# Optimization experiments

Measured on AMD Instinct MI355X. Metric: run time of the kernel, lower is better.

The kernel has to match this reference:

```python
import jax, jax.numpy as jnp
import numpy as np

N = 30000      # nodes
E = 480000     # edges
NF = 92        # node features
EF = 50        # edge features
D1 = 64        # dim1
D2 = 64        # dim2
L = 3          # conv_count
FC = 2         # fc_count
G = 256        # graphs in batch
EPS = 1e-5


def setup_inputs() -> dict:
    key = jax.random.key(0)
    ks = jax.random.split(key, 20)
    s = 0.05
    zd = 2 * D1 + EF  # CGConv concat dim
    inp = {
        "x": jax.random.normal(ks[0], (N, NF), jnp.float32),
        "edge_attr": jax.random.uniform(ks[1], (E, EF), jnp.float32),
        "lin0_w": jax.random.normal(ks[2], (NF, D1), jnp.float32) * s,
        "lin0_b": jnp.zeros((D1,), jnp.float32),
        "conv_wf": jax.random.normal(ks[3], (L, zd, D1), jnp.float32) * s,
        "conv_bf": jnp.zeros((L, D1), jnp.float32),
        "conv_ws": jax.random.normal(ks[4], (L, zd, D1), jnp.float32) * s,
        "conv_bs": jnp.zeros((L, D1), jnp.float32),
        "bn_gamma": jnp.ones((L, D1), jnp.float32),
        "bn_beta": jnp.zeros((L, D1), jnp.float32),
        "lin1_w": jax.random.normal(ks[5], (D1, D2), jnp.float32) * s,
        "lin1_b": jnp.zeros((D2,), jnp.float32),
        "fc_w": jax.random.normal(ks[6], (FC, D2, D2), jnp.float32) * s,
        "fc_b": jnp.zeros((FC, D2), jnp.float32),
        "lin2_w": jax.random.normal(ks[7], (D2, 1), jnp.float32) * s,
        "lin2_b": jnp.zeros((1,), jnp.float32),
        "edge_index": jax.random.randint(ks[8], (2, E), 0, N),
        "batch": jnp.sort(jax.random.randint(ks[9], (N,), 0, G)),
        "n_graphs": G,
    }
    return inp


def reference(x, edge_attr, lin0_w, lin0_b, conv_wf, conv_bf, conv_ws, conv_bs,
              bn_gamma, bn_beta, lin1_w, lin1_b, fc_w, fc_b, lin2_w, lin2_b,
              edge_index, batch, n_graphs):
    n = x.shape[0]
    src = edge_index[0]  # x_j (source)
    dst = edge_index[1]  # x_i (target, aggregation index)
    h = jax.nn.relu(x @ lin0_w + lin0_b)  # [N, D1]

    # per-target edge counts for mean aggregation (constant across layers)
    cnt = jax.ops.segment_sum(jnp.ones((src.shape[0],), h.dtype), dst, num_segments=n)
    cnt = jnp.maximum(cnt, 1.0)[:, None]

    for l in range(L):
        # z = [x_i || x_j || e_ij]  -> gated message sigmoid(Wf z) * softplus(Ws z)
        z = jnp.concatenate([h[dst], h[src], edge_attr], axis=-1)  # [E, 2*D1+EF]
        m = jax.nn.sigmoid(z @ conv_wf[l] + conv_bf[l]) * jax.nn.softplus(z @ conv_ws[l] + conv_bs[l])
        aggr = jax.ops.segment_sum(m, dst, num_segments=n) / cnt  # mean aggr [N, D1]
        # BatchNorm (training-mode batch stats, biased variance as in torch)
        mu = jnp.mean(aggr, axis=0)
        var = jnp.var(aggr, axis=0)
        aggr = (aggr - mu) * jax.lax.rsqrt(var + EPS) * bn_gamma[l] + bn_beta[l]
        h = jax.nn.relu(h + aggr)  # residual then outer ReLU

    # global mean pool over graphs
    gcnt = jnp.maximum(jax.ops.segment_sum(jnp.ones((n,), h.dtype), batch, num_segments=n_graphs), 1.0)[:, None]
    out = jax.ops.segment_sum(h, batch, num_segments=n_graphs) / gcnt  # [G, D1]

    out = jax.nn.relu(out @ lin1_w + lin1_b)
    for f in range(FC):
        out = jax.nn.relu(out @ fc_w[f] + fc_b[f])
    out = out @ lin2_w + lin2_b
    return out.reshape(-1)  # [G]
```

## Files before the change

### kernel.cpp

```cpp
#include <hip/hip_runtime.h>
#include <hip/hip_bf16.h>

#define N_NODES 30000
#define N_EDGES 480000
#define NFEAT 92
#define EFEAT 50
#define D1 64
#define ZD 178
#define NL 3
#define NG 256
#define BN_EPS 1e-5f
#define NTILES (N_EDGES / 16)
#define EDGE_BLOCKS 7500
#define EDGE_GRID 7504

#define LIN0_BLOCKS 512
#define CNT_BLOCKS 1875
#define WPREP_BLOCKS 96
#define SCAN_BLOCKS ((N_NODES + 255) / 256)
#define BUILD_BLOCKS 1875
#define NP_BLOCKS 1024

typedef __attribute__((ext_vector_type(8))) short bf16x8;
typedef __attribute__((ext_vector_type(8))) unsigned short u16x8;
typedef __attribute__((ext_vector_type(4))) unsigned short u16x4;
typedef __attribute__((ext_vector_type(4))) float f32x4;

static __device__ __forceinline__ unsigned short f2bf(float v) {
  __hip_bfloat16 b = __float2bfloat16(v);
  return *(unsigned short*)&b;
}
static __device__ __forceinline__ float bfu(unsigned short u) {
  union { unsigned int i; float f; } c;
  c.i = ((unsigned int)u) << 16;
  return c.f;
}

static __device__ __forceinline__ void nodeproj_body(
    int blk0, int nblk, const float* __restrict__ hin, float* __restrict__ hout,
    const float* __restrict__ wfp, const float* __restrict__ wsm,
    unsigned short* __restrict__ projd_pk, unsigned short* __restrict__ projs_pk,
    const float* __restrict__ aggr, float* __restrict__ aggr_z,
    const float* __restrict__ invc, const float* __restrict__ musum,
    const float* __restrict__ sqsum, const float* __restrict__ gamma,
    const float* __restrict__ beta, int do_bn, float (*hl)[64]) {
  const int lane = threadIdx.x & 63;
  const int w = threadIdx.x >> 6;
  const float* W = (w < 2) ? wfp : wsm;
  const int roff = (w & 1) * 64;
  float wreg[D1];
#pragma unroll
  for (int k = 0; k < D1; ++k) wreg[k] = W[(size_t)(roff + k) * D1 + lane];
  unsigned short* pk = (w & 1) ? projs_pk : projd_pk;
  const int slot = (w < 2) ? 0 : 4;
  const int poff = (lane >> 2) * 8 + (lane & 3) + slot;
  float r = 0.0f, sh = 0.0f;
  if (do_bn) {
    const float mu = musum[lane] * (1.0f / N_NODES);
    const float var = sqsum[lane] * (1.0f / N_NODES) - mu * mu;
    r = gamma[lane] * rsqrtf(var + BN_EPS);
    sh = beta[lane] - mu * r;
  }
  for (int i = blk0; i < N_NODES; i += nblk) {
    float hv = hin[(size_t)i * D1 + lane];
    if (do_bn) {
      const float av = aggr[(size_t)i * D1 + lane] * invc[i];
      hv = fmaxf(hv + fmaf(av, r, sh), 0.0f);
      if (w == 0) hout[(size_t)i * D1 + lane] = hv;
    }
    if (w == 1) aggr_z[(size_t)i * D1 + lane] = 0.0f;
    hl[w][lane] = hv;
    __builtin_amdgcn_wave_barrier();
    const float4* hr = (const float4*)&hl[w][0];
    float acc = 0.0f;
#pragma unroll
    for (int k4 = 0; k4 < D1 / 4; ++k4) {
      const float4 v = hr[k4];
      acc = fmaf(v.x, wreg[4 * k4 + 0], acc);
      acc = fmaf(v.y, wreg[4 * k4 + 1], acc);
      acc = fmaf(v.z, wreg[4 * k4 + 2], acc);
      acc = fmaf(v.w, wreg[4 * k4 + 3], acc);
    }
    pk[(size_t)i * 128 + poff] = f2bf(acc);
    __builtin_amdgcn_wave_barrier();
  }
}

extern "C" __global__ void __launch_bounds__(256)
k_init(const float* __restrict__ x, const float* __restrict__ w,
       const float* __restrict__ b, float* __restrict__ h,
       const int* __restrict__ ei, int* __restrict__ cnt,
       const float* __restrict__ conv_wf, const float* __restrict__ conv_ws,
       unsigned short* __restrict__ Bp) {
  const int blk = blockIdx.x;
  if (blk < LIN0_BLOCKS) {
    const int lane = threadIdx.x & 63;
    const int wave = (blk * 256 + threadIdx.x) >> 6;
    const int nw = (LIN0_BLOCKS * 256) >> 6;
    float wreg[NFEAT];
#pragma unroll
    for (int k = 0; k < NFEAT; ++k) wreg[k] = w[k * D1 + lane];
    const float bj = b[lane];
    for (int i = wave; i < N_NODES; i += nw) {
      const float2* xr = (const float2*)(x + (size_t)i * NFEAT);
      float acc = bj;
#pragma unroll
      for (int k = 0; k < NFEAT / 2; ++k) {
        const float2 v = xr[k];
        acc = fmaf(v.x, wreg[2 * k], acc);
        acc = fmaf(v.y, wreg[2 * k + 1], acc);
      }
      h[(size_t)i * D1 + lane] = fmaxf(acc, 0.0f);
    }
  } else if (blk < LIN0_BLOCKS + CNT_BLOCKS) {
    const int e = (blk - LIN0_BLOCKS) * 256 + threadIdx.x;
    if (e < N_EDGES) atomicAdd(&cnt[ei[N_EDGES + e]], 1);
  } else {
    const int idx = (blk - LIN0_BLOCKS - CNT_BLOCKS) * 256 + threadIdx.x;
    const int j = idx & 7;
    const int lane = (idx >> 3) & 63;
    const int frag = (idx >> 9) & 15;
    const int l = idx >> 13;
    const int n = frag & 3;
    const int t = (frag >> 2) & 1;
    const int m = frag >> 3;
    const int k = t * 32 + (lane >> 4) * 8 + j;
    const int feat = (lane & 15) * 4 + n;
    float v = 0.0f;
    if (k < EFEAT) {
      const float* W = (m == 0) ? conv_wf : conv_ws;
      v = W[(size_t)l * ZD * D1 + (size_t)(128 + k) * D1 + feat];
    }
    Bp[idx] = f2bf(v);
  }
}

extern "C" __global__ void __launch_bounds__(256)
k_scan1(const int* __restrict__ cnt, int* __restrict__ lpre, int* __restrict__ ptot) {
  const int t = threadIdx.x;
  const int idx = blockIdx.x * 256 + t;
  const int v = (idx < N_NODES) ? cnt[idx] : 0;
  __shared__ int bs[256];
  bs[t] = v;
  __syncthreads();
  for (int off = 1; off < 256; off <<= 1) {
    int u = (t >= off) ? bs[t - off] : 0;
    __syncthreads();
    bs[t] += u;
    __syncthreads();
  }
  if (idx < N_NODES) lpre[idx] = bs[t] - v;
  if (t == 255) ptot[blockIdx.x] = bs[255];
}

extern "C" __global__ void __launch_bounds__(256)
k_scan23(const int* __restrict__ cnt, const int* __restrict__ lpre,
         const int* __restrict__ ptot, const int* __restrict__ batch,
         int* __restrict__ wptr, float* __restrict__ invc,
         int* __restrict__ grp) {
  __shared__ int bs[128];
  const int t = threadIdx.x;
  if (t < 128) bs[t] = (t < SCAN_BLOCKS) ? ptot[t] : 0;
  __syncthreads();
  for (int off = 1; off < 128; off <<= 1) {
    int u = 0;
    if (t < 128 && t >= off) u = bs[t - off];
    __syncthreads();
    if (t < 128 && t >= off) bs[t] += u;
    __syncthreads();
  }
  const int idx = blockIdx.x * 256 + t;
  if (idx >= N_NODES) return;
  const int bid = idx >> 8;
  const int boff = (bid == 0) ? 0 : bs[bid - 1];
  wptr[idx] = boff + lpre[idx];
  invc[idx] = 1.0f / fmaxf((float)cnt[idx], 1.0f);
  const int bt = batch[idx];
  if (idx == 0)
    for (int g = 0; g <= bt; ++g) grp[g] = 0;
  else {
    const int pb = batch[idx - 1];
    for (int g = pb + 1; g <= bt; ++g) grp[g] = idx;
  }
  if (idx == N_NODES - 1)
    for (int g = bt + 1; g <= NG; ++g) grp[g] = N_NODES;
}

extern "C" __global__ void __launch_bounds__(256)
k_build(const int* __restrict__ ei, int* __restrict__ wptr,
        int4* __restrict__ ds4, const float* __restrict__ ea,
        unsigned short* __restrict__ eapb,
        const float* __restrict__ h0, const float* __restrict__ wfl,
        const float* __restrict__ wsl, unsigned short* __restrict__ projd_pk,
        unsigned short* __restrict__ projs_pk, float* __restrict__ aggrA) {
  __shared__ float hl4[4][64];
  if (blockIdx.x >= BUILD_BLOCKS) {
    nodeproj_body(blockIdx.x - BUILD_BLOCKS, NP_BLOCKS, h0, nullptr, wfl, wsl,
                  projd_pk, projs_pk, nullptr, aggrA, nullptr, nullptr, nullptr,
                  nullptr, nullptr, 0, hl4);
    return;
  }
  const int e0 = blockIdx.x * 256;
  const int e = e0 + threadIdx.x;
  const int d = ei[N_EDGES + e];
  const int s = ei[e];
  const int pos = atomicAdd(&wptr[d], 1);

  const int l16 = threadIdx.x & 15;
  const int sub = threadIdx.x >> 4;
#pragma unroll
  for (int r = 0; r < 16; ++r) {
    const size_t ge = e0 + r * 16 + sub;
    unsigned short o0 = 0, o1 = 0, o2 = 0, o3 = 0;
    if (l16 < 12) {
      const float4 v = *(const float4*)(ea + ge * EFEAT + l16 * 4);
      o0 = f2bf(v.x); o1 = f2bf(v.y); o2 = f2bf(v.z); o3 = f2bf(v.w);
    } else if (l16 == 12) {
      const float2 v = *(const float2*)(ea + ge * EFEAT + 48);
      o0 = f2bf(v.x); o1 = f2bf(v.y);
    }
    u16x4 st;
    st[0] = o0; st[1] = o1; st[2] = o2; st[3] = o3;
    *(u16x4*)(eapb + (ge << 6) + l16 * 4) = st;
  }

  ds4[pos] = make_int4(d, s, e, 0);
}

extern "C" __global__ void __launch_bounds__(256)
k_nodeproj(const float* __restrict__ hin, float* __restrict__ hout,
           const float* __restrict__ wfp, const float* __restrict__ wsm,
           unsigned short* __restrict__ projd_pk, unsigned short* __restrict__ projs_pk,
           const float* __restrict__ aggr, float* __restrict__ aggr_z,
           const float* __restrict__ invc,
           const float* __restrict__ musum, const float* __restrict__ sqsum,
           const float* __restrict__ gamma, const float* __restrict__ beta) {
  __shared__ float hl[4][64];
  nodeproj_body(blockIdx.x, gridDim.x, hin, hout, wfp, wsm, projd_pk, projs_pk,
                aggr, aggr_z, invc, musum, sqsum, gamma, beta, 1, hl);
}

extern "C" __global__ void __launch_bounds__(256)
k_edgemm(const unsigned short* __restrict__ projd_pk,
         const unsigned short* __restrict__ projs_pk,
         const unsigned short* __restrict__ eapb,
         const int4* __restrict__ ds4,
         const unsigned short* __restrict__ Bp,
         const float* __restrict__ bfp, const float* __restrict__ bsp,
         float* __restrict__ aggr, float* __restrict__ musum,
         float* __restrict__ sqsum) {
  const int lane = threadIdx.x & 63;
  const int wv = threadIdx.x >> 6;
  const int col = lane & 15;
  const int quad = lane >> 4;
  __shared__ float mlds[4][16][68];

  const int vbid = (blockIdx.x & 7) * 938 + (blockIdx.x >> 3);
  if (blockIdx.x == 0 && wv == 0) {
    musum[lane] = 0.0f;
    sqsum[lane] = 0.0f;
  }
  if (vbid >= EDGE_BLOCKS) return;

  const int t = vbid * 4 + wv;
  const int base = t * 16;

  int dr[4], sr[4];
#pragma unroll
  for (int r = 0; r < 4; ++r) {
    const int4 q = ds4[base + quad * 4 + r];
    dr[r] = q.x;
    sr[r] = q.y;
  }
  const int oe = ds4[base + col].z;
  const bf16x8 Af0 = *(const bf16x8*)(eapb + ((size_t)oe << 6) + quad * 8);
  const bf16x8 Af1 = *(const bf16x8*)(eapb + ((size_t)oe << 6) + 32 + quad * 8);

  bf16x8 Bf[2][2][4];
#pragma unroll
  for (int m = 0; m < 2; ++m)
#pragma unroll
    for (int tt = 0; tt < 2; ++tt)
#pragma unroll
      for (int n = 0; n < 4; ++n)
        Bf[m][tt][n] = *(const bf16x8*)(Bp + ((((m * 2 + tt) * 4 + n) * 64 + lane) * 8));

  const f32x4 bf4 = *(const f32x4*)(bfp + col * 4);
  const f32x4 bs4 = *(const f32x4*)(bsp + col * 4);

  f32x4 aF[4], aS[4];
#pragma unroll
  for (int r = 0; r < 4; ++r) {
    const int d = dr[r];
    const int s = sr[r];
    const u16x8 pd = *(const u16x8*)(projd_pk + (size_t)d * 128 + col * 8);
    const u16x8 ss = *(const u16x8*)(projs_pk + (size_t)s * 128 + col * 8);
#pragma unroll
    for (int n = 0; n < 4; ++n) {
      aF[n][r] = bfu(pd[n]) + bfu(ss[n]) + bf4[n];
      aS[n][r] = bfu(pd[n + 4]) + bfu(ss[n + 4]) + bs4[n];
    }
  }

#pragma unroll
  for (int n = 0; n < 4; ++n) {
    aF[n] = __builtin_amdgcn_mfma_f32_16x16x32_bf16(Af0, Bf[0][0][n], aF[n], 0, 0, 0);
    aF[n] = __builtin_amdgcn_mfma_f32_16x16x32_bf16(Af1, Bf[0][1][n], aF[n], 0, 0, 0);
    aS[n] = __builtin_amdgcn_mfma_f32_16x16x32_bf16(Af0, Bf[1][0][n], aS[n], 0, 0, 0);
    aS[n] = __builtin_amdgcn_mfma_f32_16x16x32_bf16(Af1, Bf[1][1][n], aS[n], 0, 0, 0);
  }

#pragma unroll
  for (int r = 0; r < 4; ++r) {
    f32x4 mv;
#pragma unroll
    for (int n = 0; n < 4; ++n) {
      const float af = aF[n][r];
      const float as = aS[n][r];
      const float sg = __builtin_amdgcn_rcpf(1.0f + __expf(-af));
      const float sp = fmaxf(as, 0.0f) + __logf(1.0f + __expf(-fabsf(as)));
      mv[n] = sg * sp;
    }
    *(f32x4*)&mlds[wv][quad * 4 + r][col * 4] = mv;
  }
  __builtin_amdgcn_wave_barrier();

  float sum = 0.0f;
  int dcur = ds4[base].x;
#pragma unroll
  for (int p = 0; p < 16; ++p) {
    sum += mlds[wv][p][lane];
    const int dnxt = (p < 15) ? ds4[base + p + 1].x : -1;
    if (dnxt != dcur) {
      atomicAdd(&aggr[(size_t)dcur * D1 + lane], sum);
      sum = 0.0f;
      dcur = dnxt;
    }
  }
}

extern "C" __global__ void __launch_bounds__(256)
k_stats(const float* __restrict__ aggr, const float* __restrict__ invc,
        float* __restrict__ musum, float* __restrict__ sqsum) {
  const int j = threadIdx.x & 63;
  const int rid = (blockIdx.x * blockDim.x + threadIdx.x) >> 6;
  const int rstr = (gridDim.x * blockDim.x) >> 6;
  float s = 0.0f, sq = 0.0f;
  for (int i = rid; i < N_NODES; i += rstr) {
    const float v = aggr[(size_t)i * D1 + j] * invc[i];
    s += v;
    sq = fmaf(v, v, sq);
  }
  __shared__ float ls[256], lq[256];
  ls[threadIdx.x] = s;
  lq[threadIdx.x] = sq;
  __syncthreads();
  if (threadIdx.x < 64) {
    s = ls[j] + ls[64 + j] + ls[128 + j] + ls[192 + j];
    sq = lq[j] + lq[64 + j] + lq[128 + j] + lq[192 + j];
    atomicAdd(&musum[j], s);
    atomicAdd(&sqsum[j], sq);
  }
}

extern "C" __global__ void __launch_bounds__(256)
k_poolmlp(const float* __restrict__ h, const float* __restrict__ aggr,
          const float* __restrict__ invc,
          const float* __restrict__ musum, const float* __restrict__ sqsum,
          const float* __restrict__ gamma, const float* __restrict__ beta,
          const int* __restrict__ grp,
          const float* __restrict__ lin1_w, const float* __restrict__ lin1_b,
          const float* __restrict__ fc_w, const float* __restrict__ fc_b,
          const float* __restrict__ lin2_w, const float* __restrict__ lin2_b,
          float* __restrict__ out) {
  const int g = blockIdx.x;
  const int lane = threadIdx.x & 63;
  const int wv = threadIdx.x >> 6;
  const float mu = musum[lane] * (1.0f / N_NODES);
  const float var = sqsum[lane] * (1.0f / N_NODES) - mu * mu;
  const float r = gamma[lane] * rsqrtf(var + BN_EPS);
  const float sh = beta[lane] - mu * r;
  const int s = grp[g], e = grp[g + 1];
  float acc = 0.0f;
  for (int i = s + wv; i < e; i += 4) {
    const float hv = h[(size_t)i * D1 + lane];
    const float av = aggr[(size_t)i * D1 + lane] * invc[i];
    acc += fmaxf(hv + fmaf(av, r, sh), 0.0f);
  }
  __shared__ float red[4][64];
  __shared__ float vin[64];
  red[wv][lane] = acc;
  __syncthreads();
  const int j = threadIdx.x;
  float v = 0.0f;
  if (j < 64) {
    const float inv = 1.0f / fmaxf((float)(e - s), 1.0f);
    v = (red[0][j] + red[1][j] + red[2][j] + red[3][j]) * inv;
  }
  for (int layer = 0; layer < 3; ++layer) {
    if (j < 64) vin[j] = v;
    __syncthreads();
    if (j < 64) {
      const float* W;
      const float* B;
      if (layer == 0) {
        W = lin1_w;
        B = lin1_b;
      } else {
        W = fc_w + (size_t)(layer - 1) * D1 * D1;
        B = fc_b + (size_t)(layer - 1) * D1;
      }
      float a2 = B[j];
#pragma unroll 16
      for (int k = 0; k < D1; ++k) a2 = fmaf(vin[k], W[k * D1 + j], a2);
      v = fmaxf(a2, 0.0f);
    }
    __syncthreads();
  }
  if (j < 64) {
    float p = v * lin2_w[j];
#pragma unroll
    for (int off = 32; off > 0; off >>= 1) p += __shfl_down(p, off);
    if (j == 0) out[g] = p + lin2_b[0];
  }
}

extern "C" void kernel_launch(void* const* d_in, const int* in_sizes, int n_in,
                              void* d_out, int out_size, void* d_ws, size_t ws_size,
                              hipStream_t stream) {
  const float* x        = (const float*)d_in[0];
  const float* ea       = (const float*)d_in[1];
  const float* lin0_w   = (const float*)d_in[2];
  const float* lin0_b   = (const float*)d_in[3];
  const float* conv_wf  = (const float*)d_in[4];
  const float* conv_bf  = (const float*)d_in[5];
  const float* conv_ws  = (const float*)d_in[6];
  const float* conv_bs  = (const float*)d_in[7];
  const float* bn_gamma = (const float*)d_in[8];
  const float* bn_beta  = (const float*)d_in[9];
  const float* lin1_w   = (const float*)d_in[10];
  const float* lin1_b   = (const float*)d_in[11];
  const float* fc_w     = (const float*)d_in[12];
  const float* fc_b     = (const float*)d_in[13];
  const float* lin2_w   = (const float*)d_in[14];
  const float* lin2_b   = (const float*)d_in[15];
  const int*   ei       = (const int*)d_in[16];
  const int*   batch    = (const int*)d_in[17];

  uintptr_t p = (uintptr_t)d_ws;
  auto alloc = [&](size_t bytes) {
    p = (p + 255) & ~(size_t)255;
    void* r = (void*)p;
    p += bytes;
    return r;
  };
  float* h0     = (float*)alloc((size_t)N_NODES * 64 * 4);
  float* h1     = (float*)alloc((size_t)N_NODES * 64 * 4);
  unsigned short* projd_pk = (unsigned short*)alloc((size_t)N_NODES * 128 * 2);
  unsigned short* projs_pk = (unsigned short*)alloc((size_t)N_NODES * 128 * 2);
  float* aggrA  = (float*)alloc((size_t)N_NODES * 64 * 4);
  float* aggrB  = (float*)alloc((size_t)N_NODES * 64 * 4);
  float* musum  = (float*)alloc(128 * 4);
  float* sqsum  = musum + 64;
  float* invc   = (float*)alloc((size_t)N_NODES * 4);
  int*   cnt    = (int*)alloc((size_t)N_NODES * 4);
  int*   lpre   = (int*)alloc((size_t)N_NODES * 4);
  int*   ptot   = (int*)alloc((size_t)SCAN_BLOCKS * 4);
  int*   wptr   = (int*)alloc((size_t)N_NODES * 4);
  int4*  ds4    = (int4*)alloc((size_t)N_EDGES * 16);
  int*   grp    = (int*)alloc((size_t)(NG + 1) * 4);
  unsigned short* eapb = (unsigned short*)alloc((size_t)N_EDGES * 64 * 2);
  unsigned short* Bp   = (unsigned short*)alloc((size_t)NL * 16 * 64 * 8 * 2);

  hipMemsetAsync(cnt, 0, N_NODES * sizeof(int), stream);
  k_init<<<LIN0_BLOCKS + CNT_BLOCKS + WPREP_BLOCKS, 256, 0, stream>>>(
      x, lin0_w, lin0_b, h0, ei, cnt, conv_wf, conv_ws, Bp);
  k_scan1<<<SCAN_BLOCKS, 256, 0, stream>>>(cnt, lpre, ptot);
  k_scan23<<<SCAN_BLOCKS, 256, 0, stream>>>(cnt, lpre, ptot, batch, wptr, invc, grp);
  k_build<<<BUILD_BLOCKS + NP_BLOCKS, 256, 0, stream>>>(
      ei, wptr, ds4, ea, eapb, h0, conv_wf, conv_ws, projd_pk, projs_pk, aggrA);

  float* aggr_of[NL] = {aggrA, aggrB, aggrA};
  const float* hin_of[NL]  = {h0, h0, h1};
  float* hout_of[NL]       = {h0, h1, h0};

  for (int l = 0; l < NL; ++l) {
    const float* wfl = conv_wf + (size_t)l * ZD * D1;
    const float* wsl = conv_ws + (size_t)l * ZD * D1;
    if (l > 0)
      k_nodeproj<<<1024, 256, 0, stream>>>(
          hin_of[l], hout_of[l], wfl, wsl, projd_pk, projs_pk,
          aggr_of[l - 1], aggr_of[l], invc, musum, sqsum,
          bn_gamma + (size_t)(l - 1) * D1, bn_beta + (size_t)(l - 1) * D1);
    k_edgemm<<<EDGE_GRID, 256, 0, stream>>>(
        projd_pk, projs_pk, eapb, ds4,
        Bp + (size_t)l * 16 * 64 * 8,
        conv_bf + (size_t)l * D1, conv_bs + (size_t)l * D1,
        aggr_of[l], musum, sqsum);
    k_stats<<<256, 256, 0, stream>>>(aggr_of[l], invc, musum, sqsum);
  }

  k_poolmlp<<<NG, 256, 0, stream>>>(h0, aggr_of[2], invc, musum, sqsum,
                                    bn_gamma + (size_t)2 * D1, bn_beta + (size_t)2 * D1,
                                    grp, lin1_w, lin1_b, fc_w, fc_b,
                                    lin2_w, lin2_b, (float*)d_out);
}
```

Before: 626.9 us.

## Split first node projection out of build kernel and break FMA dependency chains

The layer-0 node projection is pulled out of k_build into its own k_nodeproj launch with a do_bn flag, and node-projection grids go from 1024 to 2048 blocks. The dot-product loops in nodeproj and lin0 now use four independent accumulators instead of one serial FMA chain, and empty asm statements keep the weight registers from being rematerialised. This targets instruction latency and load imbalance between the fused build and projection work, at the cost of one extra kernel launch and a different floating-point summation order.

```diff
diff --git a/kernel.cpp b/kernel.cpp
--- a/kernel.cpp
+++ b/kernel.cpp
@@ -19,7 +19,7 @@
 #define WPREP_BLOCKS 96
 #define SCAN_BLOCKS ((N_NODES + 255) / 256)
 #define BUILD_BLOCKS 1875
-#define NP_BLOCKS 1024
+#define NPROJ_BLOCKS 2048
 
 typedef __attribute__((ext_vector_type(8))) short bf16x8;
 typedef __attribute__((ext_vector_type(8))) unsigned short u16x8;
@@ -51,6 +51,8 @@
   float wreg[D1];
 #pragma unroll
   for (int k = 0; k < D1; ++k) wreg[k] = W[(size_t)(roff + k) * D1 + lane];
+#pragma unroll
+  for (int k = 0; k < D1; ++k) asm volatile("" : "+v"(wreg[k]));
   unsigned short* pk = (w & 1) ? projs_pk : projd_pk;
   const int slot = (w < 2) ? 0 : 4;
   const int poff = (lane >> 2) * 8 + (lane & 3) + slot;
@@ -72,16 +74,31 @@
     hl[w][lane] = hv;
     __builtin_amdgcn_wave_barrier();
     const float4* hr = (const float4*)&hl[w][0];
-    float acc = 0.0f;
-#pragma unroll
-    for (int k4 = 0; k4 < D1 / 4; ++k4) {
-      const float4 v = hr[k4];
-      acc = fmaf(v.x, wreg[4 * k4 + 0], acc);
-      acc = fmaf(v.y, wreg[4 * k4 + 1], acc);
-      acc = fmaf(v.z, wreg[4 * k4 + 2], acc);
-      acc = fmaf(v.w, wreg[4 * k4 + 3], acc);
-    }
-    pk[(size_t)i * 128 + poff] = f2bf(acc);
+    float a0 = 0.0f, a1 = 0.0f, a2 = 0.0f, a3 = 0.0f;
+#pragma unroll
+    for (int q = 0; q < 4; ++q) {
+      const float4 v0 = hr[q * 4 + 0];
+      const float4 v1 = hr[q * 4 + 1];
+      const float4 v2 = hr[q * 4 + 2];
+      const float4 v3 = hr[q * 4 + 3];
+      a0 = fmaf(v0.x, wreg[q * 16 + 0], a0);
+      a0 = fmaf(v0.y, wreg[q * 16 + 1], a0);
+      a0 = fmaf(v0.z, wreg[q * 16 + 2], a0);
+      a0 = fmaf(v0.w, wreg[q * 16 + 3], a0);
+      a1 = fmaf(v1.x, wreg[q * 16 + 4], a1);
+      a1 = fmaf(v1.y, wreg[q * 16 + 5], a1);
+      a1 = fmaf(v1.z, wreg[q * 16 + 6], a1);
+      a1 = fmaf(v1.w, wreg[q * 16 + 7], a1);
+      a2 = fmaf(v2.x, wreg[q * 16 + 8], a2);
+      a2 = fmaf(v2.y, wreg[q * 16 + 9], a2);
+      a2 = fmaf(v2.z, wreg[q * 16 + 10], a2);
+      a2 = fmaf(v2.w, wreg[q * 16 + 11], a2);
+      a3 = fmaf(v3.x, wreg[q * 16 + 12], a3);
+      a3 = fmaf(v3.y, wreg[q * 16 + 13], a3);
+      a3 = fmaf(v3.z, wreg[q * 16 + 14], a3);
+      a3 = fmaf(v3.w, wreg[q * 16 + 15], a3);
+    }
+    pk[(size_t)i * 128 + poff] = f2bf((a0 + a1) + (a2 + a3));
     __builtin_amdgcn_wave_barrier();
   }
 }
@@ -100,17 +117,19 @@
     float wreg[NFEAT];
 #pragma unroll
     for (int k = 0; k < NFEAT; ++k) wreg[k] = w[k * D1 + lane];
+#pragma unroll
+    for (int k = 0; k < NFEAT; ++k) asm volatile("" : "+v"(wreg[k]));
     const float bj = b[lane];
     for (int i = wave; i < N_NODES; i += nw) {
       const float2* xr = (const float2*)(x + (size_t)i * NFEAT);
-      float acc = bj;
+      float accs[4] = {bj, 0.0f, 0.0f, 0.0f};
 #pragma unroll
       for (int k = 0; k < NFEAT / 2; ++k) {
         const float2 v = xr[k];
-        acc = fmaf(v.x, wreg[2 * k], acc);
-        acc = fmaf(v.y, wreg[2 * k + 1], acc);
+        accs[(2 * k) & 3] = fmaf(v.x, wreg[2 * k], accs[(2 * k) & 3]);
+        accs[(2 * k + 1) & 3] = fmaf(v.y, wreg[2 * k + 1], accs[(2 * k + 1) & 3]);
       }
-      h[(size_t)i * D1 + lane] = fmaxf(acc, 0.0f);
+      h[(size_t)i * D1 + lane] = fmaxf((accs[0] + accs[1]) + (accs[2] + accs[3]), 0.0f);
     }
   } else if (blk < LIN0_BLOCKS + CNT_BLOCKS) {
     const int e = (blk - LIN0_BLOCKS) * 256 + threadIdx.x;
@@ -189,17 +208,7 @@
 extern "C" __global__ void __launch_bounds__(256)
 k_build(const int* __restrict__ ei, int* __restrict__ wptr,
         int4* __restrict__ ds4, const float* __restrict__ ea,
-        unsigned short* __restrict__ eapb,
-        const float* __restrict__ h0, const float* __restrict__ wfl,
-        const float* __restrict__ wsl, unsigned short* __restrict__ projd_pk,
-        unsigned short* __restrict__ projs_pk, float* __restrict__ aggrA) {
-  __shared__ float hl4[4][64];
-  if (blockIdx.x >= BUILD_BLOCKS) {
-    nodeproj_body(blockIdx.x - BUILD_BLOCKS, NP_BLOCKS, h0, nullptr, wfl, wsl,
-                  projd_pk, projs_pk, nullptr, aggrA, nullptr, nullptr, nullptr,
-                  nullptr, nullptr, 0, hl4);
-    return;
-  }
+        unsigned short* __restrict__ eapb) {
   const int e0 = blockIdx.x * 256;
   const int e = e0 + threadIdx.x;
   const int d = ei[N_EDGES + e];
@@ -234,10 +243,11 @@
            const float* __restrict__ aggr, float* __restrict__ aggr_z,
            const float* __restrict__ invc,
            const float* __restrict__ musum, const float* __restrict__ sqsum,
-           const float* __restrict__ gamma, const float* __restrict__ beta) {
+           const float* __restrict__ gamma, const float* __restrict__ beta,
+           int do_bn) {
   __shared__ float hl[4][64];
   nodeproj_body(blockIdx.x, gridDim.x, hin, hout, wfp, wsm, projd_pk, projs_pk,
-                aggr, aggr_z, invc, musum, sqsum, gamma, beta, 1, hl);
+                aggr, aggr_z, invc, musum, sqsum, gamma, beta, do_bn, hl);
 }
 
 extern "C" __global__ void __launch_bounds__(256)
@@ -477,8 +487,10 @@
       x, lin0_w, lin0_b, h0, ei, cnt, conv_wf, conv_ws, Bp);
   k_scan1<<<SCAN_BLOCKS, 256, 0, stream>>>(cnt, lpre, ptot);
   k_scan23<<<SCAN_BLOCKS, 256, 0, stream>>>(cnt, lpre, ptot, batch, wptr, invc, grp);
-  k_build<<<BUILD_BLOCKS + NP_BLOCKS, 256, 0, stream>>>(
-      ei, wptr, ds4, ea, eapb, h0, conv_wf, conv_ws, projd_pk, projs_pk, aggrA);
+  k_nodeproj<<<NPROJ_BLOCKS, 256, 0, stream>>>(
+      h0, nullptr, conv_wf, conv_ws, projd_pk, projs_pk,
+      aggrA, aggrA, invc, musum, sqsum, bn_gamma, bn_beta, 0);
+  k_build<<<BUILD_BLOCKS, 256, 0, stream>>>(ei, wptr, ds4, ea, eapb);
 
   float* aggr_of[NL] = {aggrA, aggrB, aggrA};
   const float* hin_of[NL]  = {h0, h0, h1};
@@ -488,10 +500,10 @@
     const float* wfl = conv_wf + (size_t)l * ZD * D1;
     const float* wsl = conv_ws + (size_t)l * ZD * D1;
     if (l > 0)
-      k_nodeproj<<<1024, 256, 0, stream>>>(
+      k_nodeproj<<<NPROJ_BLOCKS, 256, 0, stream>>>(
           hin_of[l], hout_of[l], wfl, wsl, projd_pk, projs_pk,
           aggr_of[l - 1], aggr_of[l], invc, musum, sqsum,
-          bn_gamma + (size_t)(l - 1) * D1, bn_beta + (size_t)(l - 1) * D1);
+          bn_gamma + (size_t)(l - 1) * D1, bn_beta + (size_t)(l - 1) * D1, 1);
     k_edgemm<<<EDGE_GRID, 256, 0, stream>>>(
         projd_pk, projs_pk, eapb, ds4,
         Bp + (size_t)l * 16 * 64 * 8,
```

Measured after the change: 661.6 us. 1.06x slower.
